# Kernel optimization log

Hardware: AMD Instinct MI355X
Metric: run time of the kernel (lower is better)

Reference implementation:

```python
import jax, jax.numpy as jnp
from jax import lax
import numpy as np

B = 8; NK = 1024; S = 256; IT_M = 16; IT_R = 16; NC = 5
TH = 0.15; TEMP = 10.0; NREF = 4; BETA = 5.0
MAX_ROT = 45.0; MAX_TRANS = 1.0
BV = B * IT_M          # B_out_v
BIV = BV * IT_R        # B_in_v


def _backproject(cor, d, K):
    # cor [N,S,2] pixels, d [N,S,1] metric depth, K [N,3,3] -> 3D points [N,S,3]
    p = jnp.concatenate([cor, jnp.ones_like(cor[..., :1])], -1)
    Kinv = jnp.linalg.inv(K)
    return d * jnp.einsum('nij,nsj->nsi', Kinv, p)


def _procrustes(X, Y, w):
    # weighted Kabsch: find R,t with Y ~ R X + t.  X,Y [N,S,3], w [N,S]
    sw = w.sum(-1, keepdims=True) + 1e-8
    cx = (w[..., None] * X).sum(1) / sw
    cy = (w[..., None] * Y).sum(1) / sw
    Xc = X - cx[:, None]
    Yc = Y - cy[:, None]
    H = jnp.einsum('ns,nsi,nsj->nij', w, Xc, Yc)
    U, _, Vt = jnp.linalg.svd(H)
    V = jnp.swapaxes(Vt, -1, -2)
    Ut = jnp.swapaxes(U, -1, -2)
    det = jnp.linalg.det(jnp.matmul(V, Ut))
    # R = V diag(1,1,det) U^T  == (V with last column scaled by det) @ U^T
    Vs = jnp.concatenate([V[:, :, :2], V[:, :, 2:] * det[:, None, None]], axis=2)
    R = jnp.matmul(Vs, Ut)
    t = cy - jnp.einsum('nij,nj->ni', R, cx)
    return R, t[:, None, :]


def _resid(X, Y, R, t):
    Yp = jnp.einsum('nij,nsj->nsi', R, X) + t
    return jnp.linalg.norm(Y - Yp, axis=-1)  # [N,S]


def _forward(matches, kps0, kps1, depth0, depth1, T_0to1,
             K_color0, K_color1, Kori_color0, Kori_color1,
             sampled_idx, sampled_idx_ransac):
    f32 = kps0.dtype
    Rgt = T_0to1[:, :3, :3]
    tgt = T_0to1[:, :3, 3]
    # decode flat match index -> (kp0, kp1) indices
    idx0 = sampled_idx // NK
    idx1 = sampled_idx % NK
    bidx = jnp.repeat(jnp.arange(B), IT_M)  # [BV]
    cor0 = jnp.swapaxes(kps0, 1, 2)[bidx[:, None], idx0]   # [BV,S,2]
    cor1 = jnp.swapaxes(kps1, 1, 2)[bidx[:, None], idx1]
    d0 = jnp.swapaxes(depth0, 1, 2)[bidx[:, None], idx0]   # [BV,S,1]
    d1 = jnp.swapaxes(depth1, 1, 2)[bidx[:, None], idx1]
    X = _backproject(cor0, d0, K_color0[bidx])              # [BV,S,3]
    Y = _backproject(cor1, d1, K_color1[bidx])
    # tile over RANSAC hypotheses (matches torch tile(unsqueeze(1)).reshape)
    Xv = jnp.repeat(X, IT_R, axis=0)                        # [BIV,S,3]
    Yv = jnp.repeat(Y, IT_R, axis=0)
    inl0 = jnp.zeros((BIV, S), f32).at[jnp.arange(BIV)[:, None], sampled_idx_ransac].set(1.0)
    # ---- local refinement (no-grad in original) ----
    Xd = lax.stop_gradient(Xv)
    Yd = lax.stop_gradient(Yv)
    inl = inl0
    inl_final = inl0
    pre = jnp.full((BIV,), float(NC), f32)
    for _ in range(NREF):
        Rd, td = _procrustes(Xd, Yd, inl)
        ref = (_resid(Xd, Yd, Rd, td) < TH).astype(f32)
        improved = ref.sum(-1) > pre
        pre = jnp.where(improved, ref.sum(-1), pre)
        inl_final = jnp.where(improved[:, None], inl, inl_final)
        inl = jnp.where(improved[:, None], ref, inl)
    # ---- differentiable final fit + scoring ----
    R, t = _procrustes(Xv, Yv, lax.stop_gradient(inl_final))
    score = jax.nn.sigmoid(BETA * (1.0 - _resid(Xv, Yv, R, t) / TH)).sum(-1)  # soft inlier count [BIV]
    rep = IT_M * IT_R
    Rgt_v = jnp.repeat(Rgt, rep, axis=0)
    tgt_v = jnp.repeat(tgt, rep, axis=0)
    tr = jnp.einsum('nij,nij->n', R, Rgt_v)  # trace(R Rgt^T)
    rot_err = jnp.degrees(jnp.arccos(jnp.clip(0.5 * (tr - 1.0), -1.0 + 1e-6, 1.0 - 1e-6)))
    trans_err = jnp.linalg.norm(t[:, 0, :] - tgt_v, axis=-1)
    # soft-clipped pose losses
    loss_rot_k = (MAX_ROT * jnp.tanh(rot_err / MAX_ROT)).reshape(BV, IT_R)
    loss_trans_k = (MAX_TRANS * jnp.tanh(trans_err / MAX_TRANS)).reshape(BV, IT_R)
    wgt = jax.nn.softmax(score.reshape(BV, IT_R) / TEMP, axis=-1)
    losses_rot = (loss_rot_k * wgt).sum(-1).reshape(B, IT_M).mean(-1, keepdims=True)
    losses_trans = (loss_trans_k * wgt).sum(-1).reshape(B, IT_M).mean(-1, keepdims=True)
    return jnp.stack([losses_rot, losses_trans])  # [2,B,1]


def setup_inputs() -> dict:
    key = jax.random.key(0)
    ks = jax.random.split(key, 10)
    matches = jax.random.uniform(ks[0], (B, NK, NK)) + 1e-6
    kps0 = jax.random.uniform(ks[1], (B, 2, NK)) * 512.0
    kps1 = jax.random.uniform(ks[2], (B, 2, NK)) * 512.0
    depth0 = jax.random.uniform(ks[3], (B, 1, NK)) * 9.5 + 0.5
    depth1 = jax.random.uniform(ks[4], (B, 1, NK)) * 9.5 + 0.5
    Kc = jnp.array([[500.0, 0.0, 256.0], [0.0, 500.0, 256.0], [0.0, 0.0, 1.0]])
    K = jnp.tile(Kc, (B, 1, 1))
    A = jax.random.normal(ks[5], (B, 3, 3))
    Q, _ = jnp.linalg.qr(A)
    Q = Q * jnp.sign(jnp.linalg.det(Q))[:, None, None]  # det = +1
    tv = 0.5 * jax.random.normal(ks[6], (B, 3))
    T = jnp.zeros((B, 4, 4)).at[:, :3, :3].set(Q).at[:, :3, 3].set(tv).at[:, 3, 3].set(1.0)
    sampled_idx = jax.random.randint(ks[7], (BV, S), 0, NK * NK)
    sampled_idx_ransac = jax.random.randint(ks[8], (BIV, NC), 0, S)
    return dict(matches=matches, kps0=kps0, kps1=kps1, depth0=depth0, depth1=depth1,
                T_0to1=T, K_color0=K, K_color1=K, Kori_color0=K, Kori_color1=K,
                sampled_idx=sampled_idx, sampled_idx_ransac=sampled_idx_ransac)


def reference(matches, kps0, kps1, depth0, depth1, T_0to1, K_color0, K_color1,
              Kori_color0, Kori_color1, sampled_idx, sampled_idx_ransac):
    return _forward(matches, kps0, kps1, depth0, depth1, T_0to1, K_color0, K_color1,
                    Kori_color0, Kori_color1, sampled_idx, sampled_idx_ransac)
```

## Files before the change

kernel.cpp:

```cpp
#include <hip/hip_runtime.h>
#include <hip/hip_bf16.h>
#include <math.h>

#ifndef M_PI
#define M_PI 3.14159265358979323846
#endif

namespace mp {

constexpr int NK   = 1024;
constexpr int S    = 256;
constexpr int NREF = 4;
constexpr int BV   = 128;
constexpr int BIV  = 2048;

template <typename T>
__device__ inline T gsum(T v) {
#pragma unroll
  for (int mk = 16; mk >= 1; mk >>= 1) v += __shfl_xor(v, mk, 64);
  return v;
}

__device__ inline void inv3(const float* __restrict__ K, double Ki[3][3]) {
  double a = K[0], b = K[1], c = K[2];
  double d = K[3], e = K[4], f = K[5];
  double g = K[6], h = K[7], i = K[8];
  double A  =  (e * i - f * h);
  double Bm = -(d * i - f * g);
  double C  =  (d * h - e * g);
  double det = a * A + b * Bm + c * C;
  double inv = 1.0 / det;
  Ki[0][0] = A * inv;  Ki[0][1] = -(b * i - c * h) * inv;  Ki[0][2] =  (b * f - c * e) * inv;
  Ki[1][0] = Bm * inv; Ki[1][1] =  (a * i - c * g) * inv;  Ki[1][2] = -(a * f - c * d) * inv;
  Ki[2][0] = C * inv;  Ki[2][1] = -(a * h - b * g) * inv;  Ki[2][2] =  (a * e - b * d) * inv;
}

__device__ inline double det3(double a, double b, double c,
                              double d, double e, double f,
                              double g, double h, double i) {
  return a * (e * i - f * h) - b * (d * i - f * g) + c * (d * h - e * g);
}

__device__ inline void fitq(const double X[8][3], const double Y[8][3],
                            unsigned wm, double R[3][3], double t[3]) {
  double acc[16];
  acc[0] = (double)__popc(wm);
#pragma unroll
  for (int r = 1; r < 16; ++r) acc[r] = 0.0;
#pragma unroll
  for (int k = 0; k < 8; ++k) {
    bool w = (wm >> k) & 1u;
    double x0 = w ? X[k][0] : 0.0, x1 = w ? X[k][1] : 0.0, x2 = w ? X[k][2] : 0.0;
    double y0 = Y[k][0], y1 = Y[k][1], y2 = Y[k][2];
    acc[1] += x0; acc[2] += x1; acc[3] += x2;
    acc[4] += w ? y0 : 0.0; acc[5] += w ? y1 : 0.0; acc[6] += w ? y2 : 0.0;
    acc[7]  += x0 * y0; acc[8]  += x0 * y1; acc[9]  += x0 * y2;
    acc[10] += x1 * y0; acc[11] += x1 * y1; acc[12] += x1 * y2;
    acc[13] += x2 * y0; acc[14] += x2 * y1; acc[15] += x2 * y2;
  }
#pragma unroll
  for (int mk = 16; mk >= 1; mk >>= 1)
#pragma unroll
    for (int r = 0; r < 16; ++r) acc[r] += __shfl_xor(acc[r], mk, 64);

  double sw = acc[0];
  double rinv = 1.0 / (sw + 1e-8);
  double cx[3], cy[3];
#pragma unroll
  for (int i = 0; i < 3; ++i) { cx[i] = acc[1 + i] * rinv; cy[i] = acc[4 + i] * rinv; }
  double H[3][3];
#pragma unroll
  for (int i = 0; i < 3; ++i)
#pragma unroll
    for (int j = 0; j < 3; ++j)
      H[i][j] = acc[7 + 3 * i + j] - cx[i] * acc[4 + j] - acc[1 + i] * cy[j] +
                sw * cx[i] * cy[j];

  double k00 =  H[0][0] + H[1][1] + H[2][2];
  double k11 =  H[0][0] - H[1][1] - H[2][2];
  double k22 = -H[0][0] + H[1][1] - H[2][2];
  double k33 = -H[0][0] - H[1][1] + H[2][2];
  double k01 = H[1][2] - H[2][1];
  double k02 = H[2][0] - H[0][2];
  double k03 = H[0][1] - H[1][0];
  double k12 = H[0][1] + H[1][0];
  double k13 = H[0][2] + H[2][0];
  double k23 = H[1][2] + H[2][1];

  double e2 = (k00 * k11 - k01 * k01) + (k00 * k22 - k02 * k02) +
              (k00 * k33 - k03 * k03) + (k11 * k22 - k12 * k12) +
              (k11 * k33 - k13 * k13) + (k22 * k33 - k23 * k23);
  double e3 = det3(k00, k01, k02, k01, k11, k12, k02, k12, k22) +
              det3(k00, k01, k03, k01, k11, k13, k03, k13, k33) +
              det3(k00, k02, k03, k02, k22, k23, k03, k23, k33) +
              det3(k11, k12, k13, k12, k22, k23, k13, k23, k33);
  double M00 = det3(k11, k12, k13, k12, k22, k23, k13, k23, k33);
  double M01 = det3(k01, k12, k13, k02, k22, k23, k03, k23, k33);
  double M02 = det3(k01, k11, k13, k02, k12, k23, k03, k13, k33);
  double M03 = det3(k01, k11, k12, k02, k12, k22, k03, k13, k23);
  double e4 = k00 * M00 - k01 * M01 + k02 * M02 - k03 * M03;

  double g0 = k00 + fabs(k01) + fabs(k02) + fabs(k03);
  double g1 = k11 + fabs(k01) + fabs(k12) + fabs(k13);
  double g2 = k22 + fabs(k02) + fabs(k12) + fabs(k23);
  double g3 = k33 + fabs(k03) + fabs(k13) + fabs(k23);
  double gersh = fmax(fmax(g0, g1), fmax(g2, g3));
  double frob = sqrt(fmax(-2.0 * e2, 0.0));
  double l0 = fmax(fmin(gersh, frob), 0.0);

  float e2f = (float)e2, e3f = (float)e3, e4f = (float)e4;
  float lamf = (float)l0;
#pragma unroll
  for (int i = 0; i < 10; ++i) {
    float l2 = lamf * lamf;
    float p  = ((l2 + e2f) * lamf - e3f) * lamf + e4f;
    float pp = (4.0f * l2 + 2.0f * e2f) * lamf - e3f;
    lamf -= p / pp;
  }
  double lam = (double)lamf;
#pragma unroll
  for (int i = 0; i < 3; ++i) {
    double l2 = lam * lam;
    double p  = ((l2 + e2) * lam - e3) * lam + e4;
    double pp = (4.0 * l2 + 2.0 * e2) * lam - e3;
    lam -= p / pp;
  }

  double m00 = k00 - lam, m11 = k11 - lam, m22 = k22 - lam, m33 = k33 - lam;
  double c00 = det3(m11, k12, k13, k12, m22, k23, k13, k23, m33);
  double c01 = -det3(k01, k12, k13, k02, m22, k23, k03, k23, m33);
  double c02 = det3(k01, m11, k13, k02, k12, k23, k03, k13, m33);
  double c03 = -det3(k01, m11, k12, k02, k12, m22, k03, k13, k23);
  double c11 = det3(m00, k02, k03, k02, m22, k23, k03, k23, m33);
  double c12 = -det3(m00, k01, k03, k02, k12, k23, k03, k13, m33);
  double c13 = det3(m00, k01, k02, k02, k12, m22, k03, k13, k23);
  double c22 = det3(m00, k01, k03, k01, m11, k13, k03, k13, m33);
  double c23 = -det3(m00, k01, k02, k01, m11, k12, k03, k13, k23);
  double c33 = det3(m00, k01, k02, k01, m11, k12, k02, k12, m22);

  double a0 = fabs(c00), a1 = fabs(c11), a2 = fabs(c22), a3 = fabs(c33);
  double q0 = c00, q1 = c01, q2 = c02, q3 = c03, bb = a0;
  bool t1 = a1 > bb; bb = t1 ? a1 : bb;
  q0 = t1 ? c01 : q0; q1 = t1 ? c11 : q1; q2 = t1 ? c12 : q2; q3 = t1 ? c13 : q3;
  bool t2 = a2 > bb; bb = t2 ? a2 : bb;
  q0 = t2 ? c02 : q0; q1 = t2 ? c12 : q1; q2 = t2 ? c22 : q2; q3 = t2 ? c23 : q3;
  bool t3 = a3 > bb;
  q0 = t3 ? c03 : q0; q1 = t3 ? c13 : q1; q2 = t3 ? c23 : q2; q3 = t3 ? c33 : q3;

  double n2 = q0 * q0 + q1 * q1 + q2 * q2 + q3 * q3;
  bool ok = n2 > 1e-250;
  double qn = rsqrt(ok ? n2 : 1.0);
  double qw = ok ? q0 * qn : 1.0;
  double qx = ok ? q1 * qn : 0.0;
  double qy = ok ? q2 * qn : 0.0;
  double qz = ok ? q3 * qn : 0.0;

  R[0][0] = 1.0 - 2.0 * (qy * qy + qz * qz);
  R[0][1] = 2.0 * (qx * qy - qw * qz);
  R[0][2] = 2.0 * (qx * qz + qw * qy);
  R[1][0] = 2.0 * (qx * qy + qw * qz);
  R[1][1] = 1.0 - 2.0 * (qx * qx + qz * qz);
  R[1][2] = 2.0 * (qy * qz - qw * qx);
  R[2][0] = 2.0 * (qx * qz - qw * qy);
  R[2][1] = 2.0 * (qy * qz + qw * qx);
  R[2][2] = 1.0 - 2.0 * (qx * qx + qy * qy);
#pragma unroll
  for (int i = 0; i < 3; ++i)
    t[i] = cy[i] - (R[i][0] * cx[0] + R[i][1] * cx[1] + R[i][2] * cx[2]);
}

__global__ __launch_bounds__(64) void pose_fit_kernel(
    const float* __restrict__ kps0, const float* __restrict__ kps1,
    const float* __restrict__ depth0, const float* __restrict__ depth1,
    const float* __restrict__ T01,
    const float* __restrict__ K0, const float* __restrict__ K1,
    const int* __restrict__ sidx, const int* __restrict__ sransac,
    double* __restrict__ oscore, double* __restrict__ olr,
    double* __restrict__ olt) {
  const int blk  = blockIdx.x;
  const int lane = threadIdx.x;
  const int grp  = lane >> 5;
  const int gl   = lane & 31;
  const int m = blk * 2 + grp;
  const int v = m >> 4;
  const int b = v >> 4;

  double Ki0[3][3], Ki1[3][3];
  inv3(K0 + b * 9, Ki0);
  inv3(K1 + b * 9, Ki1);

  double X[8][3], Y[8][3];
#pragma unroll
  for (int k = 0; k < 8; ++k) {
    int s = gl + 32 * k;
    int idx = sidx[v * S + s];
    int i0 = idx >> 10;
    int i1 = idx & (NK - 1);
    double u0 = (double)kps0[b * 2 * NK + i0];
    double w0 = (double)kps0[b * 2 * NK + NK + i0];
    double d0 = (double)depth0[b * NK + i0];
    double u1 = (double)kps1[b * 2 * NK + i1];
    double w1 = (double)kps1[b * 2 * NK + NK + i1];
    double d1 = (double)depth1[b * NK + i1];
#pragma unroll
    for (int i = 0; i < 3; ++i) {
      X[k][i] = d0 * (Ki0[i][0] * u0 + Ki0[i][1] * w0 + Ki0[i][2]);
      Y[k][i] = d1 * (Ki1[i][0] * u1 + Ki1[i][1] * w1 + Ki1[i][2]);
    }
  }

  unsigned wm = 0;
#pragma unroll
  for (int c = 0; c < 5; ++c) {
    int r = sransac[m * 5 + c];
    if ((r & 31) == gl) wm |= 1u << (r >> 5);
  }

  int pre = 5;
  float Rs[9], ts[3], sqs[8];
  for (int it = 0; it < NREF; ++it) {
    double R[3][3], t[3];
    fitq(X, Y, wm, R, t);
    float r32[9] = {(float)R[0][0], (float)R[0][1], (float)R[0][2],
                    (float)R[1][0], (float)R[1][1], (float)R[1][2],
                    (float)R[2][0], (float)R[2][1], (float)R[2][2]};
    float t0 = (float)t[0], t1 = (float)t[1], t2 = (float)t[2];
    unsigned nwm = 0, band = 0;
    float sq32[8];
#pragma unroll
    for (int k = 0; k < 8; ++k) {
      float x0 = (float)X[k][0], x1 = (float)X[k][1], x2 = (float)X[k][2];
      float e0 = (float)Y[k][0] - (r32[0] * x0 + r32[1] * x1 + r32[2] * x2 + t0);
      float e1 = (float)Y[k][1] - (r32[3] * x0 + r32[4] * x1 + r32[5] * x2 + t1);
      float e2 = (float)Y[k][2] - (r32[6] * x0 + r32[7] * x1 + r32[8] * x2 + t2);
      float sq = e0 * e0 + e1 * e1 + e2 * e2;
      sq32[k] = sq;
      nwm  |= (sq < 0.0225f) ? (1u << k) : 0u;
      band |= (fabsf(sq - 0.0225f) < 1e-4f) ? (1u << k) : 0u;
    }
    if (__any(band != 0)) {
#pragma unroll
      for (int k = 0; k < 8; ++k)
        if ((band >> k) & 1u) {
          double e0 = Y[k][0] - (R[0][0] * X[k][0] + R[0][1] * X[k][1] + R[0][2] * X[k][2] + t[0]);
          double e1 = Y[k][1] - (R[1][0] * X[k][0] + R[1][1] * X[k][1] + R[1][2] * X[k][2] + t[1]);
          double e2 = Y[k][2] - (R[2][0] * X[k][0] + R[2][1] * X[k][1] + R[2][2] * X[k][2] + t[2]);
          double sqd = e0 * e0 + e1 * e1 + e2 * e2;
          nwm = (nwm & ~(1u << k)) | ((sqd < 0.0225) ? (1u << k) : 0u);
        }
    }
    int rs = gsum(__popc(nwm));
    bool imp = rs > pre;
    bool sv = (it == 0) || imp;
#pragma unroll
    for (int i = 0; i < 9; ++i) Rs[i] = sv ? r32[i] : Rs[i];
    ts[0] = sv ? t0 : ts[0]; ts[1] = sv ? t1 : ts[1]; ts[2] = sv ? t2 : ts[2];
#pragma unroll
    for (int k = 0; k < 8; ++k) sqs[k] = sv ? sq32[k] : sqs[k];
    pre = imp ? rs : pre;
    wm  = imp ? nwm : wm;
    if (!__any(imp)) break;
  }

  float sc = 0.0f;
#pragma unroll
  for (int k = 0; k < 8; ++k) {
    float r = sqrtf(sqs[k]);
    float xar = 5.0f * (1.0f - r * (1.0f / 0.15f));
    sc += 1.0f / (1.0f + __expf(-xar));
  }
  sc = gsum(sc);

  const float* Tb = T01 + b * 16;
  float tr = 0.0f;
#pragma unroll
  for (int i = 0; i < 3; ++i)
#pragma unroll
    for (int j = 0; j < 3; ++j) tr += Rs[i * 3 + j] * Tb[i * 4 + j];
  double xcl = 0.5 * ((double)tr - 1.0);
  const double lo = -1.0 + 1e-6, hi = 1.0 - 1e-6;
  xcl = xcl < lo ? lo : (xcl > hi ? hi : xcl);
  float rot_err = acosf((float)xcl) * (float)(180.0 / M_PI);
  float te0 = ts[0] - Tb[3];
  float te1 = ts[1] - Tb[7];
  float te2 = ts[2] - Tb[11];
  float terr = sqrtf(te0 * te0 + te1 * te1 + te2 * te2);
  float lr = 45.0f * tanhf(rot_err * (1.0f / 45.0f));
  float lt = tanhf(terr);

  if (gl == 0) {
    oscore[m] = (double)sc;
    olr[m] = (double)lr;
    olt[m] = (double)lt;
  }
}

__global__ __launch_bounds__(128) void pose_reduce_kernel(
    const double* __restrict__ oscore, const double* __restrict__ olr,
    const double* __restrict__ olt, float* __restrict__ out) {
  __shared__ double slr[BV], slt[BV];
  int k = threadIdx.x;
  double sc[16];
  double mx = -1e300;
#pragma unroll
  for (int r = 0; r < 16; ++r) {
    sc[r] = oscore[k * 16 + r];
    mx = fmax(mx, sc[r]);
  }
  double den = 0.0, wl = 0.0, wt = 0.0;
#pragma unroll
  for (int r = 0; r < 16; ++r) {
    double e = (double)__expf((float)((sc[r] - mx) * 0.1));
    den += e;
    wl += e * olr[k * 16 + r];
    wt += e * olt[k * 16 + r];
  }
  slr[k] = wl / den;
  slt[k] = wt / den;
  __syncthreads();
  if (k < 8) {
    double a = 0.0, c = 0.0;
#pragma unroll
    for (int i = 0; i < 16; ++i) {
      a += slr[k * 16 + i];
      c += slt[k * 16 + i];
    }
    out[k]     = (float)(a / 16.0);
    out[8 + k] = (float)(c / 16.0);
  }
}

}

extern "C" void kernel_launch(void* const* d_in, const int* in_sizes, int n_in,
                              void* d_out, int out_size, void* d_ws, size_t ws_size,
                              hipStream_t stream) {
  const float* kps0   = (const float*)d_in[1];
  const float* kps1   = (const float*)d_in[2];
  const float* depth0 = (const float*)d_in[3];
  const float* depth1 = (const float*)d_in[4];
  const float* T01    = (const float*)d_in[5];
  const float* K0     = (const float*)d_in[6];
  const float* K1     = (const float*)d_in[7];
  const int* sidx     = (const int*)d_in[10];
  const int* srans    = (const int*)d_in[11];

  double* ws     = (double*)d_ws;
  double* oscore = ws;
  double* olr    = ws + mp::BIV;
  double* olt    = ws + 2 * mp::BIV;

  mp::pose_fit_kernel<<<mp::BIV / 2, 64, 0, stream>>>(
      kps0, kps1, depth0, depth1, T01, K0, K1, sidx, srans, oscore, olr, olt);
  mp::pose_reduce_kernel<<<1, 128, 0, stream>>>(
      oscore, olr, olt, (float*)d_out);
}
```

Before: 17.01 us.

## Compute quaternion eigen-solve in fp32 and fuse final reduction via last-block atomic

Moves the 4x4 quaternion characteristic polynomial, Newton iterations and cofactor eigenvector computation from double to float, dropping the double refinement steps and using fast division. Fuses the separate softmax-weighted reduction kernel into the fit kernel: each block bumps an atomic counter and the last block does the final reduction in float. Intermediate buffers shrink from double to float. This removes most fp64 ALU work and one kernel launch, but risks accuracy on ill-conditioned fits, adds a memset launch, and adds atomic and fence overhead.

```diff
diff --git a/kernel.cpp b/kernel.cpp
--- a/kernel.cpp
+++ b/kernel.cpp
@@ -13,6 +13,7 @@
 constexpr int NREF = 4;
 constexpr int BV   = 128;
 constexpr int BIV  = 2048;
+constexpr int NBLK = BIV / 2;
 
 template <typename T>
 __device__ inline T gsum(T v) {
@@ -35,14 +36,14 @@
   Ki[2][0] = C * inv;  Ki[2][1] = -(a * h - b * g) * inv;  Ki[2][2] =  (a * e - b * d) * inv;
 }
 
-__device__ inline double det3(double a, double b, double c,
-                              double d, double e, double f,
-                              double g, double h, double i) {
+__device__ inline float det3f(float a, float b, float c,
+                              float d, float e, float f,
+                              float g, float h, float i) {
   return a * (e * i - f * h) - b * (d * i - f * g) + c * (d * h - e * g);
 }
 
 __device__ inline void fitq(const double X[8][3], const double Y[8][3],
-                            unsigned wm, double R[3][3], double t[3]) {
+                            unsigned wm, float R[9], double t[3]) {
   double acc[16];
   acc[0] = (double)__popc(wm);
 #pragma unroll
@@ -76,70 +77,60 @@
       H[i][j] = acc[7 + 3 * i + j] - cx[i] * acc[4 + j] - acc[1 + i] * cy[j] +
                 sw * cx[i] * cy[j];
 
-  double k00 =  H[0][0] + H[1][1] + H[2][2];
-  double k11 =  H[0][0] - H[1][1] - H[2][2];
-  double k22 = -H[0][0] + H[1][1] - H[2][2];
-  double k33 = -H[0][0] - H[1][1] + H[2][2];
-  double k01 = H[1][2] - H[2][1];
-  double k02 = H[2][0] - H[0][2];
-  double k03 = H[0][1] - H[1][0];
-  double k12 = H[0][1] + H[1][0];
-  double k13 = H[0][2] + H[2][0];
-  double k23 = H[1][2] + H[2][1];
-
-  double e2 = (k00 * k11 - k01 * k01) + (k00 * k22 - k02 * k02) +
-              (k00 * k33 - k03 * k03) + (k11 * k22 - k12 * k12) +
-              (k11 * k33 - k13 * k13) + (k22 * k33 - k23 * k23);
-  double e3 = det3(k00, k01, k02, k01, k11, k12, k02, k12, k22) +
-              det3(k00, k01, k03, k01, k11, k13, k03, k13, k33) +
-              det3(k00, k02, k03, k02, k22, k23, k03, k23, k33) +
-              det3(k11, k12, k13, k12, k22, k23, k13, k23, k33);
-  double M00 = det3(k11, k12, k13, k12, k22, k23, k13, k23, k33);
-  double M01 = det3(k01, k12, k13, k02, k22, k23, k03, k23, k33);
-  double M02 = det3(k01, k11, k13, k02, k12, k23, k03, k13, k33);
-  double M03 = det3(k01, k11, k12, k02, k12, k22, k03, k13, k23);
-  double e4 = k00 * M00 - k01 * M01 + k02 * M02 - k03 * M03;
-
-  double g0 = k00 + fabs(k01) + fabs(k02) + fabs(k03);
-  double g1 = k11 + fabs(k01) + fabs(k12) + fabs(k13);
-  double g2 = k22 + fabs(k02) + fabs(k12) + fabs(k23);
-  double g3 = k33 + fabs(k03) + fabs(k13) + fabs(k23);
-  double gersh = fmax(fmax(g0, g1), fmax(g2, g3));
-  double frob = sqrt(fmax(-2.0 * e2, 0.0));
-  double l0 = fmax(fmin(gersh, frob), 0.0);
-
-  float e2f = (float)e2, e3f = (float)e3, e4f = (float)e4;
-  float lamf = (float)l0;
-#pragma unroll
-  for (int i = 0; i < 10; ++i) {
-    float l2 = lamf * lamf;
-    float p  = ((l2 + e2f) * lamf - e3f) * lamf + e4f;
-    float pp = (4.0f * l2 + 2.0f * e2f) * lamf - e3f;
-    lamf -= p / pp;
-  }
-  double lam = (double)lamf;
-#pragma unroll
-  for (int i = 0; i < 3; ++i) {
-    double l2 = lam * lam;
-    double p  = ((l2 + e2) * lam - e3) * lam + e4;
-    double pp = (4.0 * l2 + 2.0 * e2) * lam - e3;
-    lam -= p / pp;
-  }
-
-  double m00 = k00 - lam, m11 = k11 - lam, m22 = k22 - lam, m33 = k33 - lam;
-  double c00 = det3(m11, k12, k13, k12, m22, k23, k13, k23, m33);
-  double c01 = -det3(k01, k12, k13, k02, m22, k23, k03, k23, m33);
-  double c02 = det3(k01, m11, k13, k02, k12, k23, k03, k13, m33);
-  double c03 = -det3(k01, m11, k12, k02, k12, m22, k03, k13, k23);
-  double c11 = det3(m00, k02, k03, k02, m22, k23, k03, k23, m33);
-  double c12 = -det3(m00, k01, k03, k02, k12, k23, k03, k13, m33);
-  double c13 = det3(m00, k01, k02, k02, k12, m22, k03, k13, k23);
-  double c22 = det3(m00, k01, k03, k01, m11, k13, k03, k13, m33);
-  double c23 = -det3(m00, k01, k02, k01, m11, k12, k03, k13, k23);
-  double c33 = det3(m00, k01, k02, k01, m11, k12, k02, k12, m22);
-
-  double a0 = fabs(c00), a1 = fabs(c11), a2 = fabs(c22), a3 = fabs(c33);
-  double q0 = c00, q1 = c01, q2 = c02, q3 = c03, bb = a0;
+  float k00 = (float)( H[0][0] + H[1][1] + H[2][2]);
+  float k11 = (float)( H[0][0] - H[1][1] - H[2][2]);
+  float k22 = (float)(-H[0][0] + H[1][1] - H[2][2]);
+  float k33 = (float)(-H[0][0] - H[1][1] + H[2][2]);
+  float k01 = (float)(H[1][2] - H[2][1]);
+  float k02 = (float)(H[2][0] - H[0][2]);
+  float k03 = (float)(H[0][1] - H[1][0]);
+  float k12 = (float)(H[0][1] + H[1][0]);
+  float k13 = (float)(H[0][2] + H[2][0]);
+  float k23 = (float)(H[1][2] + H[2][1]);
+
+  float e2 = (k00 * k11 - k01 * k01) + (k00 * k22 - k02 * k02) +
+             (k00 * k33 - k03 * k03) + (k11 * k22 - k12 * k12) +
+             (k11 * k33 - k13 * k13) + (k22 * k33 - k23 * k23);
+  float e3 = det3f(k00, k01, k02, k01, k11, k12, k02, k12, k22) +
+             det3f(k00, k01, k03, k01, k11, k13, k03, k13, k33) +
+             det3f(k00, k02, k03, k02, k22, k23, k03, k23, k33) +
+             det3f(k11, k12, k13, k12, k22, k23, k13, k23, k33);
+  float M00 = det3f(k11, k12, k13, k12, k22, k23, k13, k23, k33);
+  float M01 = det3f(k01, k12, k13, k02, k22, k23, k03, k23, k33);
+  float M02 = det3f(k01, k11, k13, k02, k12, k23, k03, k13, k33);
+  float M03 = det3f(k01, k11, k12, k02, k12, k22, k03, k13, k23);
+  float e4 = k00 * M00 - k01 * M01 + k02 * M02 - k03 * M03;
+
+  float g0 = k00 + fabsf(k01) + fabsf(k02) + fabsf(k03);
+  float g1 = k11 + fabsf(k01) + fabsf(k12) + fabsf(k13);
+  float g2 = k22 + fabsf(k02) + fabsf(k12) + fabsf(k23);
+  float g3 = k33 + fabsf(k03) + fabsf(k13) + fabsf(k23);
+  float gersh = fmaxf(fmaxf(g0, g1), fmaxf(g2, g3));
+  float frob = sqrtf(fmaxf(-2.0f * e2, 0.0f));
+  float lam = fmaxf(fminf(gersh, frob), 0.0f) * 1.00001f;
+
+#pragma unroll
+  for (int i = 0; i < 9; ++i) {
+    float l2 = lam * lam;
+    float p  = ((l2 + e2) * lam - e3) * lam + e4;
+    float pp = (4.0f * l2 + 2.0f * e2) * lam - e3;
+    lam -= __fdividef(p, pp);
+  }
+
+  float m00 = k00 - lam, m11 = k11 - lam, m22 = k22 - lam, m33 = k33 - lam;
+  float c00 = det3f(m11, k12, k13, k12, m22, k23, k13, k23, m33);
+  float c01 = -det3f(k01, k12, k13, k02, m22, k23, k03, k23, m33);
+  float c02 = det3f(k01, m11, k13, k02, k12, k23, k03, k13, m33);
+  float c03 = -det3f(k01, m11, k12, k02, k12, m22, k03, k13, k23);
+  float c11 = det3f(m00, k02, k03, k02, m22, k23, k03, k23, m33);
+  float c12 = -det3f(m00, k01, k03, k02, k12, k23, k03, k13, m33);
+  float c13 = det3f(m00, k01, k02, k02, k12, m22, k03, k13, k23);
+  float c22 = det3f(m00, k01, k03, k01, m11, k13, k03, k13, m33);
+  float c23 = -det3f(m00, k01, k02, k01, m11, k12, k03, k13, k23);
+  float c33 = det3f(m00, k01, k02, k01, m11, k12, k02, k12, m22);
+
+  float a0 = fabsf(c00), a1 = fabsf(c11), a2 = fabsf(c22), a3 = fabsf(c33);
+  float q0 = c00, q1 = c01, q2 = c02, q3 = c03, bb = a0;
   bool t1 = a1 > bb; bb = t1 ? a1 : bb;
   q0 = t1 ? c01 : q0; q1 = t1 ? c11 : q1; q2 = t1 ? c12 : q2; q3 = t1 ? c13 : q3;
   bool t2 = a2 > bb; bb = t2 ? a2 : bb;
@@ -147,36 +138,38 @@
   bool t3 = a3 > bb;
   q0 = t3 ? c03 : q0; q1 = t3 ? c13 : q1; q2 = t3 ? c23 : q2; q3 = t3 ? c33 : q3;
 
-  double n2 = q0 * q0 + q1 * q1 + q2 * q2 + q3 * q3;
-  bool ok = n2 > 1e-250;
-  double qn = rsqrt(ok ? n2 : 1.0);
-  double qw = ok ? q0 * qn : 1.0;
-  double qx = ok ? q1 * qn : 0.0;
-  double qy = ok ? q2 * qn : 0.0;
-  double qz = ok ? q3 * qn : 0.0;
-
-  R[0][0] = 1.0 - 2.0 * (qy * qy + qz * qz);
-  R[0][1] = 2.0 * (qx * qy - qw * qz);
-  R[0][2] = 2.0 * (qx * qz + qw * qy);
-  R[1][0] = 2.0 * (qx * qy + qw * qz);
-  R[1][1] = 1.0 - 2.0 * (qx * qx + qz * qz);
-  R[1][2] = 2.0 * (qy * qz - qw * qx);
-  R[2][0] = 2.0 * (qx * qz - qw * qy);
-  R[2][1] = 2.0 * (qy * qz + qw * qx);
-  R[2][2] = 1.0 - 2.0 * (qx * qx + qy * qy);
+  float n2 = q0 * q0 + q1 * q1 + q2 * q2 + q3 * q3;
+  bool ok = n2 > 1e-30f;
+  float qn = rsqrtf(ok ? n2 : 1.0f);
+  float qw = ok ? q0 * qn : 1.0f;
+  float qx = ok ? q1 * qn : 0.0f;
+  float qy = ok ? q2 * qn : 0.0f;
+  float qz = ok ? q3 * qn : 0.0f;
+
+  R[0] = 1.0f - 2.0f * (qy * qy + qz * qz);
+  R[1] = 2.0f * (qx * qy - qw * qz);
+  R[2] = 2.0f * (qx * qz + qw * qy);
+  R[3] = 2.0f * (qx * qy + qw * qz);
+  R[4] = 1.0f - 2.0f * (qx * qx + qz * qz);
+  R[5] = 2.0f * (qy * qz - qw * qx);
+  R[6] = 2.0f * (qx * qz - qw * qy);
+  R[7] = 2.0f * (qy * qz + qw * qx);
+  R[8] = 1.0f - 2.0f * (qx * qx + qy * qy);
 #pragma unroll
   for (int i = 0; i < 3; ++i)
-    t[i] = cy[i] - (R[i][0] * cx[0] + R[i][1] * cx[1] + R[i][2] * cx[2]);
-}
-
-__global__ __launch_bounds__(64) void pose_fit_kernel(
+    t[i] = cy[i] - ((double)R[3 * i] * cx[0] + (double)R[3 * i + 1] * cx[1] +
+                    (double)R[3 * i + 2] * cx[2]);
+}
+
+__global__ __launch_bounds__(64) void pose_kernel(
     const float* __restrict__ kps0, const float* __restrict__ kps1,
     const float* __restrict__ depth0, const float* __restrict__ depth1,
     const float* __restrict__ T01,
     const float* __restrict__ K0, const float* __restrict__ K1,
     const int* __restrict__ sidx, const int* __restrict__ sransac,
-    double* __restrict__ oscore, double* __restrict__ olr,
-    double* __restrict__ olt) {
+    float* __restrict__ oscore, float* __restrict__ olr,
+    float* __restrict__ olt, unsigned* __restrict__ ctr,
+    float* __restrict__ out) {
   const int blk  = blockIdx.x;
   const int lane = threadIdx.x;
   const int grp  = lane >> 5;
@@ -219,20 +212,18 @@
   int pre = 5;
   float Rs[9], ts[3], sqs[8];
   for (int it = 0; it < NREF; ++it) {
-    double R[3][3], t[3];
+    float R[9];
+    double t[3];
     fitq(X, Y, wm, R, t);
-    float r32[9] = {(float)R[0][0], (float)R[0][1], (float)R[0][2],
-                    (float)R[1][0], (float)R[1][1], (float)R[1][2],
-                    (float)R[2][0], (float)R[2][1], (float)R[2][2]};
-    float t0 = (float)t[0], t1 = (float)t[1], t2 = (float)t[2];
+    float t0 = (float)t[0], t1f = (float)t[1], t2f = (float)t[2];
     unsigned nwm = 0, band = 0;
     float sq32[8];
 #pragma unroll
     for (int k = 0; k < 8; ++k) {
       float x0 = (float)X[k][0], x1 = (float)X[k][1], x2 = (float)X[k][2];
-      float e0 = (float)Y[k][0] - (r32[0] * x0 + r32[1] * x1 + r32[2] * x2 + t0);
-      float e1 = (float)Y[k][1] - (r32[3] * x0 + r32[4] * x1 + r32[5] * x2 + t1);
-      float e2 = (float)Y[k][2] - (r32[6] * x0 + r32[7] * x1 + r32[8] * x2 + t2);
+      float e0 = (float)Y[k][0] - (R[0] * x0 + R[1] * x1 + R[2] * x2 + t0);
+      float e1 = (float)Y[k][1] - (R[3] * x0 + R[4] * x1 + R[5] * x2 + t1f);
+      float e2 = (float)Y[k][2] - (R[6] * x0 + R[7] * x1 + R[8] * x2 + t2f);
       float sq = e0 * e0 + e1 * e1 + e2 * e2;
       sq32[k] = sq;
       nwm  |= (sq < 0.0225f) ? (1u << k) : 0u;
@@ -242,9 +233,9 @@
 #pragma unroll
       for (int k = 0; k < 8; ++k)
         if ((band >> k) & 1u) {
-          double e0 = Y[k][0] - (R[0][0] * X[k][0] + R[0][1] * X[k][1] + R[0][2] * X[k][2] + t[0]);
-          double e1 = Y[k][1] - (R[1][0] * X[k][0] + R[1][1] * X[k][1] + R[1][2] * X[k][2] + t[1]);
-          double e2 = Y[k][2] - (R[2][0] * X[k][0] + R[2][1] * X[k][1] + R[2][2] * X[k][2] + t[2]);
+          double e0 = Y[k][0] - ((double)R[0] * X[k][0] + (double)R[1] * X[k][1] + (double)R[2] * X[k][2] + t[0]);
+          double e1 = Y[k][1] - ((double)R[3] * X[k][0] + (double)R[4] * X[k][1] + (double)R[5] * X[k][2] + t[1]);
+          double e2 = Y[k][2] - ((double)R[6] * X[k][0] + (double)R[7] * X[k][1] + (double)R[8] * X[k][2] + t[2]);
           double sqd = e0 * e0 + e1 * e1 + e2 * e2;
           nwm = (nwm & ~(1u << k)) | ((sqd < 0.0225) ? (1u << k) : 0u);
         }
@@ -253,8 +244,8 @@
     bool imp = rs > pre;
     bool sv = (it == 0) || imp;
 #pragma unroll
-    for (int i = 0; i < 9; ++i) Rs[i] = sv ? r32[i] : Rs[i];
-    ts[0] = sv ? t0 : ts[0]; ts[1] = sv ? t1 : ts[1]; ts[2] = sv ? t2 : ts[2];
+    for (int i = 0; i < 9; ++i) Rs[i] = sv ? R[i] : Rs[i];
+    ts[0] = sv ? t0 : ts[0]; ts[1] = sv ? t1f : ts[1]; ts[2] = sv ? t2f : ts[2];
 #pragma unroll
     for (int k = 0; k < 8; ++k) sqs[k] = sv ? sq32[k] : sqs[k];
     pre = imp ? rs : pre;
@@ -289,44 +280,50 @@
   float lt = tanhf(terr);
 
   if (gl == 0) {
-    oscore[m] = (double)sc;
-    olr[m] = (double)lr;
-    olt[m] = (double)lt;
-  }
-}
-
-__global__ __launch_bounds__(128) void pose_reduce_kernel(
-    const double* __restrict__ oscore, const double* __restrict__ olr,
-    const double* __restrict__ olt, float* __restrict__ out) {
-  __shared__ double slr[BV], slt[BV];
-  int k = threadIdx.x;
-  double sc[16];
-  double mx = -1e300;
-#pragma unroll
-  for (int r = 0; r < 16; ++r) {
-    sc[r] = oscore[k * 16 + r];
-    mx = fmax(mx, sc[r]);
-  }
-  double den = 0.0, wl = 0.0, wt = 0.0;
-#pragma unroll
-  for (int r = 0; r < 16; ++r) {
-    double e = (double)__expf((float)((sc[r] - mx) * 0.1));
-    den += e;
-    wl += e * olr[k * 16 + r];
-    wt += e * olt[k * 16 + r];
-  }
-  slr[k] = wl / den;
-  slt[k] = wt / den;
-  __syncthreads();
-  if (k < 8) {
-    double a = 0.0, c = 0.0;
-#pragma unroll
-    for (int i = 0; i < 16; ++i) {
-      a += slr[k * 16 + i];
-      c += slt[k * 16 + i];
-    }
-    out[k]     = (float)(a / 16.0);
-    out[8 + k] = (float)(c / 16.0);
+    oscore[m] = sc;
+    olr[m] = lr;
+    olt[m] = lt;
+  }
+
+  __threadfence();
+  unsigned old = 0;
+  if (lane == 0) old = atomicAdd(ctr, 1u);
+  old = (unsigned)__shfl((int)old, 0, 64);
+  if (old == NBLK - 1) {
+    __threadfence();
+    float rlr[2], rlt[2];
+#pragma unroll
+    for (int h = 0; h < 2; ++h) {
+      int row = 2 * lane + h;
+      float s[16], mx = -1e30f;
+#pragma unroll
+      for (int r = 0; r < 16; ++r) {
+        s[r] = oscore[row * 16 + r];
+        mx = fmaxf(mx, s[r]);
+      }
+      float den = 0.0f, wl = 0.0f, wt = 0.0f;
+#pragma unroll
+      for (int r = 0; r < 16; ++r) {
+        float e = __expf((s[r] - mx) * 0.1f);
+        den += e;
+        wl += e * olr[row * 16 + r];
+        wt += e * olt[row * 16 + r];
+      }
+      float di = 1.0f / den;
+      rlr[h] = wl * di;
+      rlt[h] = wt * di;
+    }
+    float a = rlr[0] + rlr[1], c = rlt[0] + rlt[1];
+#pragma unroll
+    for (int mk = 1; mk <= 4; mk <<= 1) {
+      a += __shfl_xor(a, mk, 64);
+      c += __shfl_xor(c, mk, 64);
+    }
+    if ((lane & 7) == 0) {
+      int bo = lane >> 3;
+      out[bo]     = a * (1.0f / 16.0f);
+      out[8 + bo] = c * (1.0f / 16.0f);
+    }
   }
 }
 
@@ -345,13 +342,14 @@
   const int* sidx     = (const int*)d_in[10];
   const int* srans    = (const int*)d_in[11];
 
-  double* ws     = (double*)d_ws;
-  double* oscore = ws;
-  double* olr    = ws + mp::BIV;
-  double* olt    = ws + 2 * mp::BIV;
-
-  mp::pose_fit_kernel<<<mp::BIV / 2, 64, 0, stream>>>(
-      kps0, kps1, depth0, depth1, T01, K0, K1, sidx, srans, oscore, olr, olt);
-  mp::pose_reduce_kernel<<<1, 128, 0, stream>>>(
-      oscore, olr, olt, (float*)d_out);
-}
+  float* ws      = (float*)d_ws;
+  float* oscore  = ws;
+  float* olr     = ws + mp::BIV;
+  float* olt     = ws + 2 * mp::BIV;
+  unsigned* ctr  = (unsigned*)(ws + 3 * mp::BIV);
+
+  hipMemsetAsync(ctr, 0, sizeof(unsigned), stream);
+  mp::pose_kernel<<<mp::NBLK, 64, 0, stream>>>(
+      kps0, kps1, depth0, depth1, T01, K0, K1, sidx, srans,
+      oscore, olr, olt, ctr, (float*)d_out);
+}
```

New measurement: 40.91 us. 2.4x slower.
